# Performance work log

Measured on AMD Instinct MI355X. Metric: run time of the kernel, lower is better.

The kernel has to match this reference:

```python
import jax, jax.numpy as jnp
import numpy as np

NUM_FRAMES = 257  # init_kwargs num_frames
K = 5             # number of keyframes


def setup_inputs() -> dict:
    key = jax.random.key(0)
    k1, k2, k3 = jax.random.split(key, 3)
    latents = jax.random.normal(k1, (K, 1, 128, 32, 32), dtype=jnp.float32)
    strengths = jax.random.uniform(k2, (K,), dtype=jnp.float32)
    # unique sorted frame indices in [0, NUM_FRAMES) (original skips duplicate segments)
    frame_indices = jnp.sort(
        jax.random.choice(k3, NUM_FRAMES, (K,), replace=False)
    ).astype(jnp.int32)
    return {"latents": latents, "strengths": strengths, "frame_indices": frame_indices}


def reference(latents, strengths, frame_indices):
    """Vectorized equivalent of MultiKeyframeProcessor.process_keyframes
    (interpolation_mode='linear').

    latents:       [K, B, C, H, W] sorted by frame_indices
    strengths:     [K]
    frame_indices: [K] int, sorted, unique, all < NUM_FRAMES
    Returns (conditioning_latents [B,C,T,H,W], conditioning_masks [B,T]).
    """
    T = NUM_FRAMES
    fi = frame_indices
    Kk = fi.shape[0]
    t = jnp.arange(T, dtype=jnp.int32)
    # index of last keyframe with frame_index <= t (-1 means before first keyframe)
    j = jnp.searchsorted(fi, t, side="right") - 1
    j0 = jnp.clip(j, 0, Kk - 1)
    j1 = jnp.clip(j + 1, 0, Kk - 1)

    fif = fi.astype(jnp.float32)
    tf = t.astype(jnp.float32)

    before = t < fi[0]
    after = t > fi[-1]
    at_kf = fi[j0] == t  # frame coincides with a keyframe (false when before)
    interior = ~(before | after | at_kf)

    denom = jnp.maximum(fif[j1] - fif[j0], 1.0)
    alpha = (tf - fif[j0]) / denom  # linear interpolation weight
    w1 = jnp.where(interior, alpha, 0.0)   # weight for next keyframe
    w0 = 1.0 - w1                          # weight for previous keyframe

    # --- conditioning masks (per-frame strength) ---
    m_mid = w0 * strengths[j0] + w1 * strengths[j1]  # covers interior and at_kf
    decay_before = jnp.maximum(1.0 - (fif[0] - tf) / jnp.maximum(fif[0], 1.0), 0.0)
    decay_after = jnp.maximum(1.0 - (tf - fif[-1]) / (T - fif[-1]), 0.0)
    mask_t = jnp.where(before, strengths[0] * decay_before,
             jnp.where(after, strengths[-1] * decay_after, m_mid))  # [T]

    # --- conditioning latents ---
    # before: j0==0, w1==0 -> first latent; after: j0==j1==K-1, w1==0 -> last latent
    lat0 = latents[j0]  # [T, B, C, H, W]
    lat1 = latents[j1]  # [T, B, C, H, W]
    out = w0[:, None, None, None, None] * lat0 + w1[:, None, None, None, None] * lat1
    conditioning_latents = jnp.moveaxis(out, 0, 2)  # [B, C, T, H, W]

    B = latents.shape[1]
    conditioning_masks = jnp.broadcast_to(mask_t[None, :], (B, T))
    return conditioning_latents, conditioning_masks
```

## Files before the change

kernel.cpp:

```cpp
#include <hip/hip_runtime.h>


#define T_FRAMES 257
#define KK 5
#define PER_KEY 131072
#define HW 1024
#define HW4 256
#define LAT_OUT 33685504

typedef float f32x4 __attribute__((ext_vector_type(4)));

__global__ __launch_bounds__(256) void mkp_kernel(
    const float* __restrict__ lat,
    const float* __restrict__ str,
    const int* __restrict__ fi,
    float* __restrict__ out)
{
    const int bx  = blockIdx.x;
    const int tid = threadIdx.x;
    const int c   = bx / T_FRAMES;
    const int t   = bx - c * T_FRAMES;

    int   fiv[KK];
    float sv[KK];
#pragma unroll
    for (int k = 0; k < KK; ++k) { fiv[k] = fi[k]; sv[k] = str[k]; }

    int j = -1;
#pragma unroll
    for (int k = 0; k < KK; ++k) j += (fiv[k] <= t) ? 1 : 0;
    const int j0 = max(j, 0);
    const int j1 = min(j + 1, KK - 1);

    const bool before   = t < fiv[0];
    const bool after    = t > fiv[KK - 1];
    const bool at_kf    = (fiv[j0] == t);
    const bool interior = !(before || after || at_kf);

    const float tf    = (float)t;
    const float fj0   = (float)fiv[j0];
    const float fj1   = (float)fiv[j1];
    const float denom = fmaxf(fj1 - fj0, 1.0f);
    const float alpha = (tf - fj0) / denom;
    const float w1    = interior ? alpha : 0.0f;
    const float w0    = 1.0f - w1;

    const f32x4 a = *((const f32x4*)(lat + j0 * PER_KEY + c * HW) + tid);
    const f32x4 b = *((const f32x4*)(lat + j1 * PER_KEY + c * HW) + tid);
    f32x4 r;
    r.x = w0 * a.x + w1 * b.x;
    r.y = w0 * a.y + w1 * b.y;
    r.z = w0 * a.z + w1 * b.z;
    r.w = w0 * a.w + w1 * b.w;

    __builtin_nontemporal_store(r, ((f32x4*)out) + bx * HW4 + tid);

    if (bx < T_FRAMES && tid == 0) {
        float m;
        if (before) {
            const float f0f = (float)fiv[0];
            m = sv[0] * fmaxf(1.0f - (f0f - tf) / fmaxf(f0f, 1.0f), 0.0f);
        } else if (after) {
            const float fLf = (float)fiv[KK - 1];
            m = sv[KK - 1] * fmaxf(1.0f - (tf - fLf) / ((float)T_FRAMES - fLf), 0.0f);
        } else {
            m = w0 * sv[j0] + w1 * sv[j1];
        }
        out[LAT_OUT + t] = m;
    }
}

extern "C" void kernel_launch(void* const* d_in, const int* in_sizes, int n_in,
                              void* d_out, int out_size, void* d_ws, size_t ws_size,
                              hipStream_t stream)
{
    const float* lat = (const float*)d_in[0];
    const float* str = (const float*)d_in[1];
    const int*   fi  = (const int*)d_in[2];
    float* out = (float*)d_out;

    const int grid = 128 * T_FRAMES;
    mkp_kernel<<<grid, 256, 0, stream>>>(lat, str, fi, out);
}
```

Before: 157.6 us.

## Load all keyframes once per block and loop over a span of frames

Each block now handles one channel and a group of up to 33 consecutive frames, replacing the old one-block-per-(channel, frame) grid. All five keyframe slices are loaded into registers once, and each output frame is written as a weighted sum over the five with one-hot weights. This removes repeated latent loads and per-block launch overhead, but cuts the grid to 1024 blocks and serializes up to 33 stores per thread. That may expose less memory parallelism for what is a write-bound kernel.

```diff
diff --git a/kernel.cpp b/kernel.cpp
--- a/kernel.cpp
+++ b/kernel.cpp
@@ -5,8 +5,9 @@
 #define KK 5
 #define PER_KEY 131072
 #define HW 1024
-#define HW4 256
 #define LAT_OUT 33685504
+#define TGROUPS 8
+#define TLEN 33
 
 typedef float f32x4 __attribute__((ext_vector_type(4)));
 
@@ -16,46 +17,84 @@
     const int* __restrict__ fi,
     float* __restrict__ out)
 {
-    const int bx  = blockIdx.x;
+    const int b   = blockIdx.x;
     const int tid = threadIdx.x;
-    const int c   = bx / T_FRAMES;
-    const int t   = bx - c * T_FRAMES;
+    const int g   = b >> 7;
+    const int c   = b & 127;
 
     int   fiv[KK];
     float sv[KK];
 #pragma unroll
     for (int k = 0; k < KK; ++k) { fiv[k] = fi[k]; sv[k] = str[k]; }
 
-    int j = -1;
+    f32x4 kf[KK];
 #pragma unroll
-    for (int k = 0; k < KK; ++k) j += (fiv[k] <= t) ? 1 : 0;
-    const int j0 = max(j, 0);
-    const int j1 = min(j + 1, KK - 1);
+    for (int k = 0; k < KK; ++k)
+        kf[k] = *((const f32x4*)(lat + k * PER_KEY + c * HW) + tid);
 
-    const bool before   = t < fiv[0];
-    const bool after    = t > fiv[KK - 1];
-    const bool at_kf    = (fiv[j0] == t);
-    const bool interior = !(before || after || at_kf);
+    const int t0 = g * TLEN;
+    const int t1 = (t0 + TLEN < T_FRAMES) ? t0 + TLEN : T_FRAMES;
 
-    const float tf    = (float)t;
-    const float fj0   = (float)fiv[j0];
-    const float fj1   = (float)fiv[j1];
-    const float denom = fmaxf(fj1 - fj0, 1.0f);
-    const float alpha = (tf - fj0) / denom;
-    const float w1    = interior ? alpha : 0.0f;
-    const float w0    = 1.0f - w1;
+    float* po = out + c * (T_FRAMES * HW);
 
-    const f32x4 a = *((const f32x4*)(lat + j0 * PER_KEY + c * HW) + tid);
-    const f32x4 b = *((const f32x4*)(lat + j1 * PER_KEY + c * HW) + tid);
-    f32x4 r;
-    r.x = w0 * a.x + w1 * b.x;
-    r.y = w0 * a.y + w1 * b.y;
-    r.z = w0 * a.z + w1 * b.z;
-    r.w = w0 * a.w + w1 * b.w;
+    for (int t = t0; t < t1; ++t) {
+        int j = -1;
+#pragma unroll
+        for (int k = 0; k < KK; ++k) j += (fiv[k] <= t) ? 1 : 0;
+        const int j0 = (j < 0) ? 0 : j;
+        const int j1 = (j + 1 > KK - 1) ? KK - 1 : j + 1;
 
-    __builtin_nontemporal_store(r, ((f32x4*)out) + bx * HW4 + tid);
+        const bool before   = t < fiv[0];
+        const bool after    = t > fiv[KK - 1];
+        const bool at_kf    = (fiv[j0] == t);
+        const bool interior = !(before || after || at_kf);
 
-    if (bx < T_FRAMES && tid == 0) {
+        const float tf    = (float)t;
+        const float fj0   = (float)fiv[j0];
+        const float fj1   = (float)fiv[j1];
+        const float denom = fmaxf(fj1 - fj0, 1.0f);
+        const float alpha = (tf - fj0) / denom;
+        const float w1    = interior ? alpha : 0.0f;
+        const float w0    = 1.0f - w1;
+
+        float wk[KK];
+#pragma unroll
+        for (int k = 0; k < KK; ++k)
+            wk[k] = ((k == j0) ? w0 : 0.0f) + ((k == j1) ? w1 : 0.0f);
+
+        f32x4 r = kf[0] * wk[0];
+#pragma unroll
+        for (int k = 1; k < KK; ++k) {
+            r.x = fmaf(kf[k].x, wk[k], r.x);
+            r.y = fmaf(kf[k].y, wk[k], r.y);
+            r.z = fmaf(kf[k].z, wk[k], r.z);
+            r.w = fmaf(kf[k].w, wk[k], r.w);
+        }
+
+        __builtin_nontemporal_store(r, (f32x4*)(po + t * HW) + tid);
+    }
+
+    if (c == 0 && tid < (t1 - t0)) {
+        const int t = t0 + tid;
+        int j = -1;
+#pragma unroll
+        for (int k = 0; k < KK; ++k) j += (fiv[k] <= t) ? 1 : 0;
+        const int j0 = (j < 0) ? 0 : j;
+        const int j1 = (j + 1 > KK - 1) ? KK - 1 : j + 1;
+
+        const bool before   = t < fiv[0];
+        const bool after    = t > fiv[KK - 1];
+        const bool at_kf    = (fiv[j0] == t);
+        const bool interior = !(before || after || at_kf);
+
+        const float tf    = (float)t;
+        const float fj0   = (float)fiv[j0];
+        const float fj1   = (float)fiv[j1];
+        const float denom = fmaxf(fj1 - fj0, 1.0f);
+        const float alpha = (tf - fj0) / denom;
+        const float w1    = interior ? alpha : 0.0f;
+        const float w0    = 1.0f - w1;
+
         float m;
         if (before) {
             const float f0f = (float)fiv[0];
@@ -79,6 +118,6 @@
     const int*   fi  = (const int*)d_in[2];
     float* out = (float*)d_out;
 
-    const int grid = 128 * T_FRAMES;
+    const int grid = TGROUPS * 128;
     mkp_kernel<<<grid, 256, 0, stream>>>(lat, str, fi, out);
 }
```

New measurement: 149.5 us. -5.1%, faster.
